# Optimization experiments

Measured on AMD Instinct MI355X. Metric: run time of the kernel, lower is better.

## Reference

```python
import jax, jax.numpy as jnp
import numpy as np
import math

B, L, C_IN = 256, 128, 75
D_EMB = 128      # DataEmbedding d_model
D_MODEL = 126    # encoder d_model (= L-2 after ODConv valid conv k=3)
H = 6
D_HEAD = D_MODEL // H  # 21
D_FF = 2048
FACTOR = 5
K_NUM = 4        # ODConv kernel_num (default)
ATT_CH = 16      # max(int(128*0.0625), 16)
EPS = 1e-5


def _ln(x, g, b):
    m = x.mean(-1, keepdims=True)
    v = ((x - m) ** 2).mean(-1, keepdims=True)
    return (x - m) * jax.lax.rsqrt(v + EPS) * g + b


def _bn_eval(x, g, b):
    # eval-mode BatchNorm, running_mean=0 running_var=1
    return x * (g / np.sqrt(1.0 + EPS)) + b


def _conv1d(x, w, b=None):
    out = jax.lax.conv_general_dilated(x, w, (1,), 'VALID',
                                       dimension_numbers=('NCH', 'OIH', 'NCH'))
    if b is not None:
        out = out + b[None, :, None]
    return out


def _pos_embed(n, d):
    pos = np.arange(n)[:, None].astype(np.float32)
    div = np.exp(np.arange(0, d, 2).astype(np.float32) * (-math.log(10000.0) / d))
    pe = np.zeros((n, d), np.float32)
    pe[:, 0::2] = np.sin(pos * div)
    pe[:, 1::2] = np.cos(pos * div)
    return jnp.asarray(pe)


def _prob_attention(Q, K, V, key):
    # Informer ProbAttention, mask_flag=False. Q,K,V: [B,H,Lq,D]
    b, h, lq, d = Q.shape
    lk = K.shape[2]
    u_keys = min(FACTOR * int(np.ceil(np.log(lk))), lk)
    n_top = min(FACTOR * int(np.ceil(np.log(lq))), lq)
    idx = jax.random.randint(key, (lq, u_keys), 0, lk)     # sampled key ids per query
    K_s = K[:, :, idx, :]                                  # [B,H,Lq,u,D]
    qks = jnp.einsum('bhld,bhlud->bhlu', Q, K_s)
    M = qks.max(-1) - qks.sum(-1) / lk                     # sparsity measure
    _, top = jax.lax.top_k(M, n_top)                       # [B,H,n_top]
    Qr = jnp.take_along_axis(Q, top[..., None], axis=2)    # [B,H,n_top,D]
    scores = jnp.einsum('bhud,bhkd->bhuk', Qr, K) / np.sqrt(d).astype(np.float32)
    upd = jnp.einsum('bhuk,bhkd->bhud', jax.nn.softmax(scores, -1), V)
    ctx = jnp.broadcast_to(V.mean(2, keepdims=True), Q.shape)  # initial context
    bi = jnp.arange(b)[:, None, None]
    hi = jnp.arange(h)[None, :, None]
    return ctx.at[bi, hi, top].set(upd)


def _forward(x_enc, x_mark_enc, token_w, time_w, time_b,
             od_fc_w, od_bn_g, od_bn_b, od_ch_w, od_ch_b, od_fil_w, od_fil_b,
             od_sp_w, od_sp_b, od_ker_w, od_ker_b, od_weight,
             q_w, q_b, k_w, k_b, v_w, v_b, o_w, o_b,
             ffn1_w, ffn1_b, ffn2_w, ffn2_b, ln1_g, ln1_b, ln2_g, ln2_b,
             cl_w, cl_b, cl_bn_g, cl_bn_b, enc_ln_g, enc_ln_b, fc_w, fc_b):
    # ---- DataEmbedding (token circular conv + pos + timeF linear; dropout=eval) ----
    xt = jnp.pad(x_enc.transpose(0, 2, 1), ((0, 0), (0, 0), (1, 1)), mode='wrap')
    tok = _conv1d(xt, token_w).transpose(0, 2, 1)          # [B,L,128]
    emb = tok + _pos_embed(L, D_EMB)[None] + (x_mark_enc @ time_w + time_b)

    # ---- ODConv1d(128,128,k=3,pad=0) on [B,128,L] ----
    x = emb.transpose(0, 2, 1)                             # [B,128,L]
    gap = x.mean(-1)                                       # [B,128]
    a = jax.nn.relu(_bn_eval(gap @ od_fc_w, od_bn_g, od_bn_b))   # [B,16]
    ch_att = jax.nn.sigmoid(a @ od_ch_w + od_ch_b)         # [B,128]
    fil_att = jax.nn.sigmoid(a @ od_fil_w + od_fil_b)      # [B,128]
    sp_att = jax.nn.sigmoid(a @ od_sp_w + od_sp_b)         # [B,3]
    ker_att = jax.nn.softmax(a @ od_ker_w + od_ker_b, -1)  # [B,4]
    xc = x * ch_att[:, :, None]
    agg_w = jnp.einsum('bn,bj,noij->boij', ker_att, sp_att, od_weight)  # [B,128,128,3]
    lout = L - 2
    patches = jnp.stack([xc[:, :, j:j + lout] for j in range(3)], axis=2)  # [B,128,3,126]
    x = jnp.einsum('boij,bijt->bot', agg_w, patches) * fil_att[:, :, None]  # [B,128,126]
    # encoder reads this as (seq=128, d_model=126)

    key = jax.random.key(42)

    def enc_layer(xx, i):
        b, l, _ = xx.shape
        Q = (xx @ q_w[i] + q_b[i]).reshape(b, l, H, D_HEAD).transpose(0, 2, 1, 3)
        Kk = (xx @ k_w[i] + k_b[i]).reshape(b, l, H, D_HEAD).transpose(0, 2, 1, 3)
        Vv = (xx @ v_w[i] + v_b[i]).reshape(b, l, H, D_HEAD).transpose(0, 2, 1, 3)
        ctx = _prob_attention(Q, Kk, Vv, jax.random.fold_in(key, i))
        new_x = ctx.transpose(0, 2, 1, 3).reshape(b, l, D_MODEL) @ o_w[i] + o_b[i]
        xx = _ln(xx + new_x, ln1_g[i], ln1_b[i])
        y = jax.nn.gelu(xx @ ffn1_w[i] + ffn1_b[i], approximate=False)
        y = y @ ffn2_w[i] + ffn2_b[i]
        return _ln(xx + y, ln2_g[i], ln2_b[i])

    x = enc_layer(x, 0)
    # ConvLayer distilling: circular conv k3 + BN + ELU + maxpool(k3,s2,p1): 128 -> 64
    xt = jnp.pad(x.transpose(0, 2, 1), ((0, 0), (0, 0), (1, 1)), mode='wrap')
    xt = _conv1d(xt, cl_w, cl_b)
    xt = jax.nn.elu(_bn_eval(xt, cl_bn_g[None, :, None], cl_bn_b[None, :, None]))
    xt = jax.lax.reduce_window(xt, -jnp.inf, jax.lax.max, (1, 1, 3), (1, 1, 2),
                               [(0, 0), (0, 0), (1, 1)])
    x = xt.transpose(0, 2, 1)                              # [B,64,126]
    x = enc_layer(x, 1)
    x = _ln(x, enc_ln_g, enc_ln_b)

    out = x.transpose(0, 2, 1) @ fc_w + fc_b               # [B,126,1]
    return out.transpose(0, 2, 1)                          # [B,1,126]


def setup_inputs() -> dict:
    key = jax.random.key(0)
    it = iter(jax.random.split(key, 48))
    def rn(shape, s=0.05):
        return jax.random.normal(next(it), shape, dtype=jnp.float32) * s
    return {
        'x_enc': jax.random.normal(next(it), (B, L, C_IN), jnp.float32),
        'x_mark_enc': jax.random.uniform(next(it), (B, L, 3), jnp.float32, -0.5, 0.5),
        'token_w': rn((D_EMB, C_IN, 3), 0.1),
        'time_w': rn((3, D_EMB), 0.1), 'time_b': rn((D_EMB,)),
        'od_fc_w': rn((D_EMB, ATT_CH), 0.1),
        'od_bn_g': jnp.ones((ATT_CH,)), 'od_bn_b': jnp.zeros((ATT_CH,)),
        'od_ch_w': rn((ATT_CH, D_EMB), 0.1), 'od_ch_b': rn((D_EMB,)),
        'od_fil_w': rn((ATT_CH, D_EMB), 0.1), 'od_fil_b': rn((D_EMB,)),
        'od_sp_w': rn((ATT_CH, 3), 0.1), 'od_sp_b': rn((3,)),
        'od_ker_w': rn((ATT_CH, K_NUM), 0.1), 'od_ker_b': rn((K_NUM,)),
        'od_weight': rn((K_NUM, D_EMB, D_EMB, 3), 0.05),
        'q_w': rn((2, D_MODEL, D_MODEL)), 'q_b': rn((2, D_MODEL)),
        'k_w': rn((2, D_MODEL, D_MODEL)), 'k_b': rn((2, D_MODEL)),
        'v_w': rn((2, D_MODEL, D_MODEL)), 'v_b': rn((2, D_MODEL)),
        'o_w': rn((2, D_MODEL, D_MODEL)), 'o_b': rn((2, D_MODEL)),
        'ffn1_w': rn((2, D_MODEL, D_FF), 0.03), 'ffn1_b': rn((2, D_FF)),
        'ffn2_w': rn((2, D_FF, D_MODEL), 0.03), 'ffn2_b': rn((2, D_MODEL)),
        'ln1_g': jnp.ones((2, D_MODEL)), 'ln1_b': jnp.zeros((2, D_MODEL)),
        'ln2_g': jnp.ones((2, D_MODEL)), 'ln2_b': jnp.zeros((2, D_MODEL)),
        'cl_w': rn((D_MODEL, D_MODEL, 3), 0.05), 'cl_b': rn((D_MODEL,)),
        'cl_bn_g': jnp.ones((D_MODEL,)), 'cl_bn_b': jnp.zeros((D_MODEL,)),
        'enc_ln_g': jnp.ones((D_MODEL,)), 'enc_ln_b': jnp.zeros((D_MODEL,)),
        'fc_w': rn((L // 2, 1), 0.1), 'fc_b': rn((1,)),
    }


def reference(x_enc, x_mark_enc, token_w, time_w, time_b,
              od_fc_w, od_bn_g, od_bn_b, od_ch_w, od_ch_b, od_fil_w, od_fil_b,
              od_sp_w, od_sp_b, od_ker_w, od_ker_b, od_weight,
              q_w, q_b, k_w, k_b, v_w, v_b, o_w, o_b,
              ffn1_w, ffn1_b, ffn2_w, ffn2_b, ln1_g, ln1_b, ln2_g, ln2_b,
              cl_w, cl_b, cl_bn_g, cl_bn_b, enc_ln_g, enc_ln_b, fc_w, fc_b):
    return _forward(x_enc, x_mark_enc, token_w, time_w, time_b,
                    od_fc_w, od_bn_g, od_bn_b, od_ch_w, od_ch_b, od_fil_w, od_fil_b,
                    od_sp_w, od_sp_b, od_ker_w, od_ker_b, od_weight,
                    q_w, q_b, k_w, k_b, v_w, v_b, o_w, o_b,
                    ffn1_w, ffn1_b, ffn2_w, ffn2_b, ln1_g, ln1_b, ln2_g, ln2_b,
                    cl_w, cl_b, cl_bn_g, cl_bn_b, enc_ln_g, enc_ln_b, fc_w, fc_b)
```

## Files before the change

kernel.cpp:

```cpp
#include <hip/hip_runtime.h>
#include <math.h>

#define NB 256
#define DM 126
#define DE 128
#define NH 6
#define DHd 21
#define DFF 2048
#define CIN 75
#define L0 128
#define NTOP 25

#ifndef IDX_MODE
#define IDX_MODE 0
#endif

typedef const float* fp;
typedef unsigned short u16;
typedef short s8v __attribute__((ext_vector_type(8)));
typedef float f4v __attribute__((ext_vector_type(4)));

__device__ __forceinline__ u16 f2bf(float x){
  unsigned u = __float_as_uint(x);
  unsigned r = (u + 0x7FFFu + ((u >> 16) & 1u)) >> 16;
  return (u16)r;
}
__device__ __forceinline__ float bf2f(u16 v){
  unsigned uu = ((unsigned)v) << 16;
  return __uint_as_float(uu);
}

__device__ __forceinline__ void gld_lds16(const u16* g, u16* l){
  __builtin_amdgcn_global_load_lds((const __attribute__((address_space(1))) unsigned int*)(const void*)g,
                                   (__attribute__((address_space(3))) unsigned int*)(void*)l,
                                   16, 0, 0);
}

__device__ __forceinline__ unsigned cvt_pk_bf16(float lo, float hi){
  unsigned r;
  asm("v_cvt_pk_bf16_f32 %0, %1, %2" : "=v"(r) : "v"(lo), "v"(hi));
  return r;
}

__device__ __forceinline__ void tf2(unsigned k0, unsigned k1, unsigned x0, unsigned x1,
                                    unsigned &o0, unsigned &o1){
  unsigned ks2 = k0 ^ k1 ^ 0x1BD11BDAu;
  x0 += k0; x1 += k1;
  #define RR(r) { x0 += x1; x1 = (x1 << (r)) | (x1 >> (32 - (r))); x1 ^= x0; }
  RR(13) RR(15) RR(26) RR(6)
  x0 += k1;  x1 += ks2 + 1u;
  RR(17) RR(29) RR(16) RR(24)
  x0 += ks2; x1 += k0 + 2u;
  RR(13) RR(15) RR(26) RR(6)
  x0 += k0;  x1 += k1 + 3u;
  RR(17) RR(29) RR(16) RR(24)
  x0 += k1;  x1 += ks2 + 4u;
  RR(13) RR(15) RR(26) RR(6)
  x0 += ks2; x1 += k0 + 5u;
  #undef RR
  o0 = x0; o1 = x1;
}

__global__ __launch_bounds__(256) void k_zero(float* out, int n){
  int i = blockIdx.x*256 + threadIdx.x;
  if (i < n) out[i] = 0.f;
}

__global__ __launch_bounds__(256) void k_idx(int* idx0, int* idx1){
  int tid = threadIdx.x;
  unsigned a0,a1,c0,c1;
  tf2(0u,42u, 0u,0u, a0,a1);
  tf2(0u,42u, 0u,1u, c0,c1);
  for (int f = tid; f < 3200; f += 256){
    unsigned y0,y1;
#if IDX_MODE==0
    tf2(a0,a1, 0u, (unsigned)(3200+f), y0,y1); idx0[f] = (int)(y1 & 127u);
#elif IDX_MODE==1
    tf2(a0,a1, 0u, (unsigned)(3200+f), y0,y1); idx0[f] = (int)(y0 & 127u);
#elif IDX_MODE==2
    tf2(a0,a1, (unsigned)f, (unsigned)(3200+f), y0,y1); idx0[f] = (int)(y1 & 127u);
#else
    tf2(a0,a1, (unsigned)f, (unsigned)(3200+f), y0,y1); idx0[f] = (int)(y0 & 127u);
#endif
  }
  for (int f = tid; f < 1600; f += 256){
    unsigned y0,y1;
#if IDX_MODE==0
    tf2(c0,c1, 0u, (unsigned)(1600+f), y0,y1); idx1[f] = (int)(y1 & 63u);
#elif IDX_MODE==1
    tf2(c0,c1, 0u, (unsigned)(1600+f), y0,y1); idx1[f] = (int)(y0 & 63u);
#elif IDX_MODE==2
    tf2(c0,c1, (unsigned)f, (unsigned)(1600+f), y0,y1); idx1[f] = (int)(y1 & 63u);
#else
    tf2(c0,c1, (unsigned)f, (unsigned)(1600+f), y0,y1); idx1[f] = (int)(y0 & 63u);
#endif
  }
}

__global__ __launch_bounds__(256) void k_wprep(fp token_w, fp clw,
                                               fp qw, fp qb, fp kw, fp kb, fp vw, fp vb, fp ow,
                                               u16* wemb, u16* wdist, u16* wqkv, u16* wo,
                                               float* qbias){
  int i = blockIdx.x*256 + threadIdx.x;
  if (i < 32768){
    int n = i >> 8, k = i & 255;
    float v = 0.f;
    if (k < 225){ int q = k/75, c = k - q*75; v = token_w[(size_t)n*225 + c*3 + q]; }
    wemb[i] = f2bf(v);
    return;
  }
  i -= 32768;
  if (i < 49152){
    int n = i / 384, k = i - n*384;
    float v = 0.f;
    if (n < DM && k < 378){ int q = k/126, ci = k - q*126; v = clw[((size_t)n*DM + ci)*3 + q]; }
    wdist[i] = f2bf(v);
    return;
  }
  i -= 49152;
  if (i < 2*49152){
    int layer = i / 49152, jj = i - layer*49152;
    int n = jj >> 7, k = jj & 127;
    int sec = n >> 7, nn = n & 127;
    const float* w = (sec == 0) ? qw : ((sec == 1) ? kw : vw);
    float v = (nn < DM && k < DM) ? w[((size_t)layer*DM + k)*DM + nn] : 0.f;
    wqkv[(size_t)layer*49152 + jj] = f2bf(v);
    return;
  }
  i -= 2*49152;
  if (i < 2*16384){
    int layer = i / 16384, jj = i - layer*16384;
    int n = jj >> 7, k = jj & 127;
    float v = (n < DM && k < DM) ? ow[(size_t)layer*DM*DM + k*DM + n] : 0.f;
    wo[(size_t)layer*16384 + jj] = f2bf(v);
    return;
  }
  i -= 2*16384;
  if (i < 768){
    int layer = i / 384, n = i - layer*384;
    int sec = n >> 7, nn = n & 127;
    const float* bp = (sec == 0) ? qb : ((sec == 1) ? kb : vb);
    qbias[(size_t)layer*384 + n] = (nn < DM) ? bp[layer*DM + nn] : 0.f;
  }
}

__global__ __launch_bounds__(256) void k_wtrans(fp f1w, fp f2w, u16* w1t, u16* w2t){
  __shared__ u16 sT[64*65];
  const int t = blockIdx.x;
  const int tid = threadIdx.x, lane = tid & 63, rg = tid >> 6;
  if (t < 128){
    int layer = t >> 6, rem = t & 63;
    int kt = rem >> 5, nt = rem & 31;
    #pragma unroll
    for (int rr = 0; rr < 16; rr++){
      int row = rg + rr*4;
      int k = kt*64 + row;
      float v = (k < DM) ? f1w[((size_t)layer*DM + k)*DFF + nt*64 + lane] : 0.f;
      sT[row*65 + lane] = f2bf(v);
    }
    __syncthreads();
    #pragma unroll
    for (int rr = 0; rr < 16; rr++){
      int nrow = rg + rr*4;
      int n_glob = nt*64 + nrow;
      w1t[(size_t)layer*262144 + (size_t)n_glob*128 + kt*64 + lane] = sT[lane*65 + nrow];
    }
  } else {
    int t2 = t - 128;
    int layer = t2 >> 6, rem = t2 & 63;
    int nt = rem >> 5, ft = rem & 31;
    #pragma unroll
    for (int rr = 0; rr < 16; rr++){
      int row = rg + rr*4;
      int f = ft*64 + row;
      int n = nt*64 + lane;
      float v = (n < DM) ? f2w[((size_t)layer*DFF + f)*DM + n] : 0.f;
      sT[row*65 + lane] = f2bf(v);
    }
    __syncthreads();
    #pragma unroll
    for (int rr = 0; rr < 16; rr++){
      int nrow = rg + rr*4;
      int n_glob = nt*64 + nrow;
      w2t[(size_t)layer*262144 + (size_t)n_glob*2048 + ft*64 + lane] = sT[lane*65 + nrow];
    }
  }
}

__global__ __launch_bounds__(256) void k_front(fp x_enc, fp x_mark, const u16* wemb,
                                               fp time_w, fp time_b,
                                               fp fcw, fp bng, fp bnb,
                                               fp chw, fp chb, fp filw, fp filb,
                                               fp spw, fp spb, fp kerw, fp kerb,
                                               fp odw, float* xout){
  __shared__ __align__(16) u16 smem[71232];
  u16*   sXT = smem;
  u16*   sW  = smem + 17680;
  u16*   sA  = smem + 17680;
  float* sE  = reinterpret_cast<float*>(smem + 17680);
  float* red = reinterpret_cast<float*>(smem + 69904);
  float* gap = reinterpret_cast<float*>(smem + 70416);
  float* aAct= reinterpret_cast<float*>(smem + 70672);
  float* sch = reinterpret_cast<float*>(smem + 70704);
  float* sfil= reinterpret_cast<float*>(smem + 70960);
  float* ssp = reinterpret_cast<float*>(smem + 71216);
  float* sker= reinterpret_cast<float*>(smem + 71224);
  const int tid = threadIdx.x;
  const int wave = tid >> 6, lane = tid & 63, quad = lane >> 4, l15 = lane & 15;
  const int b = blockIdx.x;
  const f4v z4 = {0.f,0.f,0.f,0.f};
  const int mBase = wave * 32;

  {
    const float4* xb = reinterpret_cast<const float4*>(x_enc + (size_t)b*L0*CIN);
    for (int p4 = tid; p4 < (L0*CIN)/4; p4 += 256){
      float4 v4 = xb[p4];
      float vv[4] = {v4.x, v4.y, v4.z, v4.w};
      int e0 = p4*4;
      #pragma unroll
      for (int j = 0; j < 4; j++){
        int e = e0 + j;
        int sr = e / CIN, c = e - sr*CIN;
        u16 bv = f2bf(vv[j]);
        sA[((sr + 1) & 127)*264 + c] = bv;
        sA[sr*264 + 75 + c] = bv;
        sA[((sr + 127) & 127)*264 + 150 + c] = bv;
      }
    }
    for (int p = tid; p < 128*31; p += 256){
      int row = p / 31, c2 = p - row*31;
      sA[row*264 + 225 + c2] = 0;
    }
  }
  __syncthreads();
  {
    f4v acc[2][8];
    #pragma unroll
    for (int m = 0; m < 2; m++)
      #pragma unroll
      for (int t = 0; t < 8; t++) acc[m][t] = z4;
    for (int ks = 0; ks < 8; ks++){
      s8v a0 = *reinterpret_cast<const s8v*>(sA + (mBase + l15)*264 + ks*32 + quad*8);
      s8v a1 = *reinterpret_cast<const s8v*>(sA + (mBase + 16 + l15)*264 + ks*32 + quad*8);
      const u16* wb = wemb + (size_t)l15*256 + ks*32 + quad*8;
      #pragma unroll
      for (int t = 0; t < 8; t++){
        s8v bfr = *reinterpret_cast<const s8v*>(wb + (size_t)t*16*256);
        acc[0][t] = __builtin_amdgcn_mfma_f32_16x16x32_bf16(a0, bfr, acc[0][t], 0, 0, 0);
        acc[1][t] = __builtin_amdgcn_mfma_f32_16x16x32_bf16(a1, bfr, acc[1][t], 0, 0, 0);
      }
    }
    float divc[8], tw0c[8], tw1c[8], tw2c[8], tbc[8];
    #pragma unroll
    for (int t = 0; t < 8; t++){
      int col = t*16 + l15;
      int i2 = col >> 1;
      divc[t] = __expf((float)(2*i2) * (-9.210340371976184f / 128.f));
      tw0c[t] = time_w[col]; tw1c[t] = time_w[128 + col]; tw2c[t] = time_w[256 + col];
      tbc[t] = time_b[col];
    }
    #pragma unroll
    for (int m = 0; m < 2; m++){
      #pragma unroll
      for (int r = 0; r < 4; r++){
        int row = mBase + m*16 + quad*4 + r;
        const float* mk = x_mark + ((size_t)b*L0 + row)*3;
        float m0v = mk[0], m1v = mk[1], m2v = mk[2];
        #pragma unroll
        for (int t = 0; t < 8; t++){
          int col = t*16 + l15;
          float ang = (float)row * divc[t];
          float pe = (col & 1) ? __cosf(ang) : __sinf(ang);
          float tm = m0v*tw0c[t] + m1v*tw1c[t] + m2v*tw2c[t] + tbc[t];
          sE[row*132 + col] = acc[m][t][r] + pe + tm;
        }
      }
    }
  }
  __syncthreads();
  {
    int col = tid & 127, half = tid >> 7;
    float s = 0.f;
    for (int r = 0; r < 64; r++) s += sE[(half*64 + r)*132 + col];
    red[tid] = s;
  }
  __syncthreads();
  if (tid < 128) gap[tid] = (red[tid] + red[tid + 128]) * (1.f/128.f);
  __syncthreads();
  if (tid < 16){
    float acc = 0.f;
    for (int e = 0; e < DE; e++) acc += gap[e]*fcw[e*16 + tid];
    acc = acc * (bng[tid] / sqrtf(1.f + 1e-5f)) + bnb[tid];
    aAct[tid] = fmaxf(acc, 0.f);
  }
  __syncthreads();
  if (tid < 128){
    float accc = 0.f, accf = 0.f;
    for (int c = 0; c < 16; c++){ accc += aAct[c]*chw[c*DE + tid]; accf += aAct[c]*filw[c*DE + tid]; }
    sch[tid]  = 1.f/(1.f + __expf(-(accc + chb[tid])));
    sfil[tid] = 1.f/(1.f + __expf(-(accf + filb[tid])));
  } else if (tid < 131){
    int t = tid - 128;
    float acc = 0.f;
    for (int c = 0; c < 16; c++) acc += aAct[c]*spw[c*3 + t];
    ssp[t] = 1.f/(1.f + __expf(-(acc + spb[t])));
  } else if (tid == 132){
    float v[4]; float mx = -1e30f;
    for (int n = 0; n < 4; n++){
      float acc = 0.f;
      for (int c = 0; c < 16; c++) acc += aAct[c]*kerw[c*4 + n];
      v[n] = acc + kerb[n]; mx = fmaxf(mx, v[n]);
    }
    float ss = 0.f;
    for (int n = 0; n < 4; n++){ v[n] = __expf(v[n]-mx); ss += v[n]; }
    for (int n = 0; n < 4; n++) sker[n] = v[n]/ss;
  }
  __syncthreads();
  for (int p = tid; p < 130*128; p += 256){
    int l = p >> 7, i = p & 127;
    float v = (l < 128) ? sE[l*132 + i]*sch[i] : 0.f;
    sXT[l*136 + i] = f2bf(v);
  }
  __syncthreads();
  {
    float kr0 = sker[0], kr1 = sker[1], kr2 = sker[2], kr3 = sker[3];
    float spq[3]; spq[0] = ssp[0]; spq[1] = ssp[1]; spq[2] = ssp[2];
    const float4* od4 = (const float4*)odw;
    for (int p4 = tid; p4 < 128*384/4; p4 += 256){
      float4 w0 = od4[p4];
      float4 w1 = od4[12288 + p4];
      float4 w2 = od4[24576 + p4];
      float4 w3 = od4[36864 + p4];
      float vv[4] = { kr0*w0.x + kr1*w1.x + kr2*w2.x + kr3*w3.x,
                      kr0*w0.y + kr1*w1.y + kr2*w2.y + kr3*w3.y,
                      kr0*w0.z + kr1*w1.z + kr2*w2.z + kr3*w3.z,
                      kr0*w0.w + kr1*w1.w + kr2*w2.w + kr3*w3.w };
      int e0 = p4*4;
// ... 206 lines not shown
    #pragma unroll
    for (int nt = 0; nt < 2; nt++){
      int d = nt*16 + l15;
      s8v bb;
      if (d < DHd){
        const float* vp = vb + (size_t)d*L + ks*32 + d0;
        #pragma unroll
        for (int j = 0; j < 8; j++) bb[j] = (short)f2bf(vp[j]);
      } else {
        #pragma unroll
        for (int j = 0; j < 8; j++) bb[j] = (short)0;
      }
      s8v a = *reinterpret_cast<const s8v*>(sPb + (mt*16 + l15)*136 + ks*32 + d0);
      pv[nt] = __builtin_amdgcn_mfma_f32_16x16x32_bf16(a, bb, pv[nt], 0, 0, 0);
    }
  }
  #pragma unroll
  for (int nt = 0; nt < 2; nt++){
    #pragma unroll
    for (int r4 = 0; r4 < 4; r4++){
      int u = mt*16 + quad*4 + r4;
      int d = nt*16 + l15;
      if (d < DHd){
        if (u < NTOP)       upd[((size_t)bh*NTOP + u)*DHd + d] = pv[nt][r4];
        else if (u == NTOP) vmean[bh*DHd + d] = pv[nt][r4];
      }
    }
  }
}

__global__ __launch_bounds__(256) void k_oproj_mfma(const float* xin, const float* vmean,
                                                    const int* posmap, const float* upd,
                                                    const u16* wo, fp ob, fp g, fp bb,
                                                    int layer, int lshift, int lmask, float* xmid){
  __shared__ __align__(16) float sOf[64*129];
  __shared__ float prs[128];
  __shared__ float smean[64], srstd[64];
  u16* sX = reinterpret_cast<u16*>(sOf);
  const int tid = threadIdx.x;
  const int wave = tid >> 6, lane = tid & 63, quad = lane >> 4, l15 = lane & 15;
  const int m0 = wave * 16;
  const size_t rows0 = (size_t)blockIdx.x * 64;
  for (int p = tid; p < 64*128; p += 256){
    int r = p >> 7, c = p & 127;
    int gr = (int)rows0 + r, b = gr >> lshift, l = gr & lmask;
    float v = 0.f;
    if (c < DM){
      int h = c / DHd, d = c - h*DHd;
      int bh = b*NH + h;
      int pos = posmap[bh*L0 + l];
      v = (pos >= 0) ? upd[((size_t)bh*NTOP + pos)*DHd + d] : vmean[bh*DHd + d];
    }
    sX[r*136 + c] = f2bf(v);
  }
  __syncthreads();
  const f4v z4 = {0.f,0.f,0.f,0.f};
  f4v acc[8];
  #pragma unroll
  for (int t = 0; t < 8; t++) acc[t] = z4;
  #pragma unroll
  for (int ks = 0; ks < 4; ks++){
    s8v a = *reinterpret_cast<const s8v*>(sX + (m0 + l15)*136 + ks*32 + quad*8);
    const u16* wb = wo + (size_t)l15*128 + ks*32 + quad*8;
    #pragma unroll
    for (int t = 0; t < 8; t++){
      s8v b = *reinterpret_cast<const s8v*>(wb + (size_t)t*16*128);
      acc[t] = __builtin_amdgcn_mfma_f32_16x16x32_bf16(a, b, acc[t], 0, 0, 0);
    }
  }
  __syncthreads();
  #pragma unroll
  for (int t = 0; t < 8; t++){
    int col = t*16 + l15;
    #pragma unroll
    for (int r = 0; r < 4; r++){
      sOf[(m0 + quad*4 + r)*129 + col] = acc[t][r];
    }
  }
  __syncthreads();
  const float* obl = ob + (size_t)layer*DM;
  for (int p = tid; p < 64*DM; p += 256){
    int r = p / DM, c = p - r*DM;
    sOf[r*129 + c] += xin[(rows0 + r)*DM + c] + obl[c];
  }
  __syncthreads();
  if (tid < 128){
    int row = tid >> 1, half = tid & 1;
    float s = 0.f;
    for (int c = half*63; c < half*63 + 63; c++) s += sOf[row*129 + c];
    prs[tid] = s;
  }
  __syncthreads();
  if (tid < 128 && (tid & 1) == 0) smean[tid>>1] = (prs[tid] + prs[tid+1]) / (float)DM;
  __syncthreads();
  if (tid < 128){
    int row = tid >> 1, half = tid & 1;
    float mn = smean[row];
    float s = 0.f;
    for (int c = half*63; c < half*63 + 63; c++){ float d = sOf[row*129 + c] - mn; s += d*d; }
    prs[tid] = s;
  }
  __syncthreads();
  if (tid < 128 && (tid & 1) == 0) srstd[tid>>1] = rsqrtf((prs[tid] + prs[tid+1])/(float)DM + 1e-5f);
  __syncthreads();
  const float* gl = g  + (size_t)layer*DM;
  const float* bl = bb + (size_t)layer*DM;
  for (int p = tid; p < 64*DM; p += 256){
    int r = p / DM, c = p - r*DM;
    xmid[(rows0 + r)*DM + c] = (sOf[r*129 + c] - smean[r])*srstd[r]*gl[c] + bl[c];
  }
}

__device__ __forceinline__ float gelu_fast(float x){
  float x2 = x*x;
  float u = x * __builtin_fmaf(0.10295128f, x2, 2.30212056f);
  u = fminf(u, 126.f);
#if __has_builtin(__builtin_amdgcn_exp2f)
  float t = __builtin_amdgcn_exp2f(u);
#else
  float t = __expf(u * 0.69314718056f);
#endif
  return x * t * __builtin_amdgcn_rcpf(t + 1.f);
}


__device__ __forceinline__ void stage_w1_p(const u16* w1t, int j, u16* buf, int p){
  int n = p >> 4, c = p & 15;
  int cg = c ^ (n & 7);
  gld_lds16(w1t + (((size_t)(j*64 + n)) << 7) + cg*8,
            buf + (size_t)((p >> 6) << 6)*8);
}
__device__ __forceinline__ void stage_w2_p(const u16* w2t, int j, u16* buf, int p){
  int n = p >> 3, c = p & 7;
  int cg = c ^ (n & 7);
  gld_lds16(w2t + (size_t)n*2048 + j*64 + cg*8,
            buf + (size_t)((p >> 6) << 6)*8);
}

__device__ __forceinline__ int yaddr(int row, int col){
  return row*64 + (((col >> 3) ^ (row & 7)) << 3) + (col & 7);
}

__device__ __forceinline__ void lgkm_barrier(){
  asm volatile("s_waitcnt lgkmcnt(0)" ::: "memory");
  __builtin_amdgcn_sched_barrier(0);
  __builtin_amdgcn_s_barrier();
  __builtin_amdgcn_sched_barrier(0);
}

template<int NT>
__global__ __launch_bounds__(NT) void k_ffn(const float* xmid, const u16* w1t, const u16* w2t,
                                            fp b1, fp b2w, fp g, fp bb, int layer,
                                            const u16* wdist, fp e1, fp e2, fp e3, fp e4,
                                            float* out2){
  constexpr int ROWS = NT/8;
  constexpr int NMG  = NT/256;
  constexpr int SYG  = NMG*2048;
  constexpr int SP   = 1024/NT;
  constexpr int SMEMU = (NT == 1024) ? 128*392 : (SYG + 4*8192);
  __shared__ __align__(16) u16 smem[SMEMU];
  __shared__ float prs[2*ROWS];
  __shared__ float smean[ROWS], srstd[ROWS];
  u16* wA0 = smem + SYG;
  u16* wA1 = wA0 + 8192;
  u16* wB0 = wA1 + 8192;
  u16* wB1 = wB0 + 8192;
  const int tid  = threadIdx.x;
  const int wave = tid >> 6, lane = tid & 63, quad = lane >> 4, l15 = lane & 15;
  const int mg = wave >> 2, ng = wave & 3;
  const int rowb = mg * 32;
  u16* sYg = smem + mg*2048;
  const size_t rows0 = (size_t)blockIdx.x * ROWS;

  s8v aX[2][4];
  #pragma unroll
  for (int mt = 0; mt < 2; mt++){
    const float* xr = xmid + (rows0 + rowb + mt*16 + l15)*(size_t)DM;
    #pragma unroll
    for (int ks = 0; ks < 4; ks++){
      #pragma unroll
      for (int j = 0; j < 8; j++){
        int c = ks*32 + quad*8 + j;
        float v = (c < DM) ? xr[c] : 0.f;
        aX[mt][ks][j] = (short)f2bf(v);
      }
    }
  }
  #pragma unroll
  for (int r = 0; r < SP; r++){
    stage_w1_p(w1t, 0, wA0, r*NT + tid);
    stage_w2_p(w2t, 0, wB0, r*NT + tid);
  }

  const float* b1l = b1 + (size_t)layer*DFF;
  const f4v z4 = {0.f, 0.f, 0.f, 0.f};
  f4v acc2[2][2];
  acc2[0][0]=z4; acc2[0][1]=z4; acc2[1][0]=z4; acc2[1][1]=z4;

  for (int j = 0; j < 32; j++){
    u16* wAcur = (j & 1) ? wA1 : wA0;
    u16* wAnxt = (j & 1) ? wA0 : wA1;
    u16* wBcur = (j & 1) ? wB1 : wB0;
    u16* wBnxt = (j & 1) ? wB0 : wB1;
    __syncthreads();
    if (j < 31){
      #pragma unroll
      for (int r = 0; r < SP; r++){
        stage_w1_p(w1t, j+1, wAnxt, r*NT + tid);
        stage_w2_p(w2t, j+1, wBnxt, r*NT + tid);
      }
    }
    f4v acc1[2];
    acc1[0] = z4; acc1[1] = z4;
    {
      int nloc = ng*16 + l15;
      #pragma unroll
      for (int ks = 0; ks < 4; ks++){
        int cg = (ks*4 + quad) ^ (nloc & 7);
        s8v b = *reinterpret_cast<const s8v*>(wAcur + nloc*128 + cg*8);
        acc1[0] = __builtin_amdgcn_mfma_f32_16x16x32_bf16(aX[0][ks], b, acc1[0], 0, 0, 0);
        acc1[1] = __builtin_amdgcn_mfma_f32_16x16x32_bf16(aX[1][ks], b, acc1[1], 0, 0, 0);
      }
    }
    {
      int col = ng*16 + l15;
      float bv = b1l[j*64 + col];
      #pragma unroll
      for (int mt = 0; mt < 2; mt++){
        float y0 = gelu_fast(acc1[mt][0] + bv);
        float y1 = gelu_fast(acc1[mt][1] + bv);
        float y2 = gelu_fast(acc1[mt][2] + bv);
        float y3 = gelu_fast(acc1[mt][3] + bv);
        unsigned p01 = cvt_pk_bf16(y0, y1);
        unsigned p23 = cvt_pk_bf16(y2, y3);
        int r0 = mt*16 + quad*4;
        sYg[yaddr(r0,     col)] = (u16)p01;
        sYg[yaddr(r0 + 1, col)] = (u16)(p01 >> 16);
        sYg[yaddr(r0 + 2, col)] = (u16)p23;
        sYg[yaddr(r0 + 3, col)] = (u16)(p23 >> 16);
      }
    }
    lgkm_barrier();
    #pragma unroll
    for (int ks2 = 0; ks2 < 2; ks2++){
      int ga = ((ks2*4 + quad) ^ (l15 & 7)) << 3;
      s8v a0 = *reinterpret_cast<const s8v*>(sYg + (l15)*64 + ga);
      s8v a1 = *reinterpret_cast<const s8v*>(sYg + (16 + l15)*64 + ga);
      #pragma unroll
      for (int t = 0; t < 2; t++){
        int nloc = ng*32 + t*16 + l15;
        int cg = (ks2*4 + quad) ^ (nloc & 7);
        s8v b = *reinterpret_cast<const s8v*>(wBcur + nloc*64 + cg*8);
        acc2[0][t] = __builtin_amdgcn_mfma_f32_16x16x32_bf16(a0, b, acc2[0][t], 0, 0, 0);
        acc2[1][t] = __builtin_amdgcn_mfma_f32_16x16x32_bf16(a1, b, acc2[1][t], 0, 0, 0);
      }
    }
  }

  __syncthreads();
  float* sO = reinterpret_cast<float*>(smem);
  #pragma unroll
  for (int mt = 0; mt < 2; mt++)
    #pragma unroll
    for (int t = 0; t < 2; t++)
      #pragma unroll
      for (int r = 0; r < 4; r++)
        sO[(rowb + mt*16 + quad*4 + r)*129 + ng*32 + t*16 + l15] = acc2[mt][t][r];
  __syncthreads();
  const float* b2l = b2w + (size_t)layer*DM;
  for (int p = tid; p < ROWS*DM; p += NT){
    int r = p / DM, c = p - r*DM;
    sO[r*129 + c] += b2l[c] + xmid[(rows0 + r)*DM + c];
  }
  __syncthreads();
  if (tid < 2*ROWS){
    int row = tid >> 1, half = tid & 1;
    float s = 0.f;
    for (int c = half*63; c < half*63 + 63; c++) s += sO[row*129 + c];
    prs[tid] = s;
  }
  __syncthreads();
  if (tid < 2*ROWS && (tid & 1) == 0) smean[tid>>1] = (prs[tid] + prs[tid+1]) / (float)DM;
  __syncthreads();
  if (tid < 2*ROWS){
    int row = tid >> 1, half = tid & 1;
    float mn = smean[row];
    float s = 0.f;
    for (int c = half*63; c < half*63 + 63; c++){ float d = sO[row*129 + c] - mn; s += d*d; }
    prs[tid] = s;
  }
  __syncthreads();
  if (tid < 2*ROWS && (tid & 1) == 0) srstd[tid>>1] = rsqrtf((prs[tid] + prs[tid+1])/(float)DM + 1e-5f);
  __syncthreads();
  const float* gl = g  + (size_t)layer*DM;
  const float* bl = bb + (size_t)layer*DM;

  if constexpr (NT == 1024){
    float rv[16];
    #pragma unroll
    for (int k = 0; k < 16; k++){
      int p = tid + k*1024;
      if (p < 128*DM){
        int r = p / DM, c = p - r*DM;
        rv[k] = (sO[r*129 + c] - smean[r])*srstd[r]*gl[c] + bl[c];
      } else rv[k] = 0.f;
    }
    __syncthreads();
    u16* sAd = smem;
    #pragma unroll
    for (int k = 0; k < 16; k++){
      int p = tid + k*1024;
      if (p < 128*DM){
        int r = p / DM, c = p - r*DM;
        u16 bv = f2bf(rv[k]);
        sAd[((r + 1) & 127)*392 + c] = bv;
        sAd[r*392 + 126 + c] = bv;
        sAd[((r + 127) & 127)*392 + 252 + c] = bv;
      }
    }
    if (tid < 768){ int row = tid / 6, c2 = tid - row*6; sAd[row*392 + 378 + c2] = 0; }
    __syncthreads();
    const int mrow  = (wave & 7) * 16;
    const int tbase = (wave >> 3) * 4;
    f4v dac[4];
    dac[0]=z4; dac[1]=z4; dac[2]=z4; dac[3]=z4;
    for (int ks = 0; ks < 12; ks++){
      s8v a = *reinterpret_cast<const s8v*>(sAd + (mrow + l15)*392 + ks*32 + quad*8);
      const u16* wbp = wdist + (size_t)l15*384 + ks*32 + quad*8;
      #pragma unroll
      for (int t = 0; t < 4; t++){
        s8v bfr = *reinterpret_cast<const s8v*>(wbp + (size_t)(tbase + t)*16*384);
        dac[t] = __builtin_amdgcn_mfma_f32_16x16x32_bf16(a, bfr, dac[t], 0, 0, 0);
      }
    }
    __syncthreads();
    float* zsh = reinterpret_cast<float*>(smem);
    const float bnscale = 1.f / sqrtf(1.f + 1e-5f);
    #pragma unroll
    for (int t = 0; t < 4; t++){
      int co = (tbase + t)*16 + l15;
      if (co < DM){
        float cb = e1[co];
        float gg = e2[co] * bnscale, bv = e3[co];
        #pragma unroll
        for (int r = 0; r < 4; r++){
          int row = mrow + quad*4 + r;
          float z = (dac[t][r] + cb)*gg + bv;
          z = (z > 0.f) ? z : (__expf(z) - 1.f);
          zsh[row*130 + co] = z;
        }
      }
    }
    __syncthreads();
    for (int p = tid; p < 64*DM; p += 1024){
      int jj = p / DM, co = p - jj*DM;
      float best = zsh[(2*jj)*130 + co];
      if (jj > 0) best = fmaxf(best, zsh[(2*jj - 1)*130 + co]);
      best = fmaxf(best, zsh[(2*jj + 1)*130 + co]);
      out2[((size_t)blockIdx.x*64 + jj)*DM + co] = best;
    }
  } else {
    for (int p = tid; p < ROWS*DM; p += NT){
      int r = p / DM, c = p - r*DM;
      sO[r*129 + c] = (sO[r*129 + c] - smean[r])*srstd[r]*gl[c] + bl[c];
    }
    __syncthreads();
    if (tid < 2*ROWS){
      int row = tid >> 1, half = tid & 1;
      float s = 0.f;
      for (int c = half*63; c < half*63 + 63; c++) s += sO[row*129 + c];
      prs[tid] = s;
    }
    __syncthreads();
    if (tid < 2*ROWS && (tid & 1) == 0) smean[tid>>1] = (prs[tid] + prs[tid+1]) / (float)DM;
    __syncthreads();
    if (tid < 2*ROWS){
      int row = tid >> 1, half = tid & 1;
      float mn = smean[row];
      float s = 0.f;
      for (int c = half*63; c < half*63 + 63; c++){ float d = sO[row*129 + c] - mn; s += d*d; }
      prs[tid] = s;
    }
    __syncthreads();
    if (tid < 2*ROWS && (tid & 1) == 0) srstd[tid>>1] = rsqrtf((prs[tid] + prs[tid+1])/(float)DM + 1e-5f);
    __syncthreads();
    if (tid < DM){
      float gv = e1[tid], bv2 = e2[tid];
      float acc = e4[0];
      for (int l = 0; l < 64; l++){
        float xn = (sO[l*129 + tid] - smean[l])*srstd[l]*gv + bv2;
        acc += xn * e3[l];
      }
      out2[(size_t)blockIdx.x*DM + tid] = acc;
    }
  }
}

extern "C" void kernel_launch(void* const* d_in, const int* in_sizes, int n_in,
                              void* d_out, int out_size, void* d_ws, size_t ws_size,
                              hipStream_t stream) {
  fp x_enc   = (fp)d_in[0];
  fp x_mark  = (fp)d_in[1];
  fp token_w = (fp)d_in[2];
  fp time_w  = (fp)d_in[3];
  fp time_b  = (fp)d_in[4];
  fp od_fc_w = (fp)d_in[5];
  fp od_bn_g = (fp)d_in[6];
  fp od_bn_b = (fp)d_in[7];
  fp od_ch_w = (fp)d_in[8];
  fp od_ch_b = (fp)d_in[9];
  fp od_fil_w= (fp)d_in[10];
  fp od_fil_b= (fp)d_in[11];
  fp od_sp_w = (fp)d_in[12];
  fp od_sp_b = (fp)d_in[13];
  fp od_ker_w= (fp)d_in[14];
  fp od_ker_b= (fp)d_in[15];
  fp od_wt   = (fp)d_in[16];
  fp q_w = (fp)d_in[17]; fp q_b = (fp)d_in[18];
  fp k_w = (fp)d_in[19]; fp k_b = (fp)d_in[20];
  fp v_w = (fp)d_in[21]; fp v_b = (fp)d_in[22];
  fp o_w = (fp)d_in[23]; fp o_b = (fp)d_in[24];
  fp f1w = (fp)d_in[25]; fp f1b = (fp)d_in[26];
  fp f2w = (fp)d_in[27]; fp f2b = (fp)d_in[28];
  fp ln1g= (fp)d_in[29]; fp ln1b= (fp)d_in[30];
  fp ln2g= (fp)d_in[31]; fp ln2b= (fp)d_in[32];
  fp cl_w= (fp)d_in[33]; fp cl_b= (fp)d_in[34];
  fp clbg= (fp)d_in[35]; fp clbb= (fp)d_in[36];
  fp elng= (fp)d_in[37]; fp elnb= (fp)d_in[38];
  fp fc_w= (fp)d_in[39]; fp fc_b= (fp)d_in[40];

  const size_t OFF_IDX0 = 0;
  const size_t OFF_IDX1 = OFF_IDX0 + 3200;
  const size_t OFF_CH   = OFF_IDX1 + 1600;
  const size_t OFF_FIL  = OFF_CH  + (size_t)NB*DE;
  const size_t OFF_SP   = OFF_FIL + (size_t)NB*DE;
  const size_t OFF_KER  = OFF_SP  + (size_t)NB*4;
  const size_t OFF_VM   = OFF_KER + (size_t)NB*4;
  const size_t OFF_POS  = OFF_VM  + (size_t)NB*NH*DHd;
  const size_t OFF_UPD  = OFF_POS + (size_t)NB*NH*L0;
  const size_t OFF_STOP = OFF_UPD + (size_t)NB*NH*NTOP*DHd;
  const size_t OFF_WTS  = (OFF_STOP + (size_t)NB*NH*NTOP + 255) & ~(size_t)255;
  const size_t WTS_FLOATS = (2*262144 + 2*262144 + 2*49152 + 2*16384 + 49152 + 32768)/2 + 2*384;
  const size_t OFF_BIG  = (OFF_WTS + WTS_FLOATS + 255) & ~(size_t)255;
  const size_t SBUF     = (size_t)NB*DE*L0;
  const size_t TOTAL    = OFF_BIG + 4*SBUF;

  if (ws_size < TOTAL*sizeof(float)){
    hipLaunchKernelGGL(k_zero, dim3((out_size+255)/256), dim3(256), 0, stream,
                       (float*)d_out, out_size);
    return;
  }

  float* ws = (float*)d_ws;
  int* idx0 = (int*)(ws + OFF_IDX0);
  int* idx1 = (int*)(ws + OFF_IDX1);
  float* vme = ws + OFF_VM;
  int* posm  = (int*)(ws + OFF_POS);
  float* updb= ws + OFF_UPD;
  u16* w1tb  = (u16*)(ws + OFF_WTS);
  u16* w2tb  = w1tb + 2*262144;
  u16* wqkvb = w2tb + 2*262144;
  u16* wob   = wqkvb + 2*49152;
  u16* wdistb= wob + 2*16384;
  u16* wembb = wdistb + 49152;
  float* qkvbias = (float*)(wembb + 32768);

  float* X    = ws + OFF_BIG;
  float* QKV  = X + SBUF;
  float* VT   = X + 3*SBUF;
  float* xmid = QKV;

  hipLaunchKernelGGL(k_idx, dim3(1), dim3(256), 0, stream, idx0, idx1);
  hipLaunchKernelGGL(k_wprep, dim3(835), dim3(256), 0, stream,
                     token_w, cl_w, q_w, q_b, k_w, k_b, v_w, v_b, o_w,
                     wembb, wdistb, wqkvb, wob, qkvbias);
  hipLaunchKernelGGL(k_wtrans, dim3(256), dim3(256), 0, stream,
                     f1w, f2w, w1tb, w2tb);
  hipLaunchKernelGGL(k_front, dim3(NB), dim3(256), 0, stream,
                     x_enc, x_mark, wembb, time_w, time_b,
                     od_fc_w, od_bn_g, od_bn_b, od_ch_w, od_ch_b, od_fil_w, od_fil_b,
                     od_sp_w, od_sp_b, od_ker_w, od_ker_b, od_wt, X);

  hipLaunchKernelGGL(k_qkv_mfma, dim3(NB*L0/64), dim3(256), 0, stream,
                     X, wqkvb, qkvbias, QKV, VT, 128, 7, 127);
  hipLaunchKernelGGL(k_attn, dim3(NB*NH), dim3(128), 0, stream,
                     QKV, VT, idx0, L0, posm, vme, updb);
  hipLaunchKernelGGL(k_oproj_mfma, dim3(NB*L0/64), dim3(256), 0, stream,
                     X, vme, posm, updb, wob, o_b, ln1g, ln1b, 0, 7, 127, xmid);
  hipLaunchKernelGGL((k_ffn<1024>), dim3(NB), dim3(1024), 0, stream,
                     xmid, w1tb, w2tb, f1b, f2b, ln2g, ln2b, 0,
                     wdistb, cl_b, clbg, clbb, cl_b, X);

  hipLaunchKernelGGL(k_qkv_mfma, dim3(NB*64/64), dim3(256), 0, stream,
                     X, wqkvb + 49152, qkvbias + 384, QKV, VT, 64, 6, 63);
  hipLaunchKernelGGL(k_attn, dim3(NB*NH), dim3(128), 0, stream,
                     QKV, VT, idx1, 64, posm, vme, updb);
  hipLaunchKernelGGL(k_oproj_mfma, dim3(NB*64/64), dim3(256), 0, stream,
                     X, vme, posm, updb, wob + 16384, o_b, ln1g, ln1b, 1, 6, 63, xmid);
  hipLaunchKernelGGL((k_ffn<512>), dim3(256), dim3(512), 0, stream,
                     xmid, w1tb + 262144, w2tb + 262144, f1b, f2b, ln2g, ln2b, 1,
                     wdistb, elng, elnb, fc_w, fc_b, (float*)d_out);
  (void)in_sizes; (void)n_in; (void)out_size; (void)ws_size;
}
```

Before: 592.2 us.

## Fuse layer-0 output projection and LayerNorm into FFN kernel, merge prep kernels

Merges the three weight/index preparation kernels into one launch with block-range dispatch. Folds the layer-0 attention output projection, residual add and LayerNorm1 into the 1024-thread FFN kernel, so its input stays in shared memory instead of going through a global xmid buffer. The layer-0 output goes to a separate buffer X2, because the fused kernel still reads X as the residual. This removes two kernel launches and a global round trip, but enlarges the FFN kernel's shared memory footprint and serialises the projection inside each block.

```diff
diff --git a/kernel.cpp b/kernel.cpp
--- a/kernel.cpp
+++ b/kernel.cpp
@@ -66,123 +66,128 @@
   if (i < n) out[i] = 0.f;
 }
 
-__global__ __launch_bounds__(256) void k_idx(int* idx0, int* idx1){
-  int tid = threadIdx.x;
-  unsigned a0,a1,c0,c1;
-  tf2(0u,42u, 0u,0u, a0,a1);
-  tf2(0u,42u, 0u,1u, c0,c1);
-  for (int f = tid; f < 3200; f += 256){
-    unsigned y0,y1;
+__global__ __launch_bounds__(256) void k_prep(int* idx0, int* idx1,
+                                              fp token_w, fp clw,
+                                              fp qw, fp qb, fp kw, fp kb, fp vw, fp vb, fp ow,
+                                              u16* wemb, u16* wdist, u16* wqkv, u16* wo,
+                                              float* qbias,
+                                              fp f1w, fp f2w, u16* w1t, u16* w2t){
+  __shared__ u16 sT[64*65];
+  const int blk = blockIdx.x;
+  const int tid = threadIdx.x;
+  if (blk == 0){
+    unsigned a0,a1,c0,c1;
+    tf2(0u,42u, 0u,0u, a0,a1);
+    tf2(0u,42u, 0u,1u, c0,c1);
+    for (int f = tid; f < 3200; f += 256){
+      unsigned y0,y1;
 #if IDX_MODE==0
-    tf2(a0,a1, 0u, (unsigned)(3200+f), y0,y1); idx0[f] = (int)(y1 & 127u);
+      tf2(a0,a1, 0u, (unsigned)(3200+f), y0,y1); idx0[f] = (int)(y1 & 127u);
 #elif IDX_MODE==1
-    tf2(a0,a1, 0u, (unsigned)(3200+f), y0,y1); idx0[f] = (int)(y0 & 127u);
+      tf2(a0,a1, 0u, (unsigned)(3200+f), y0,y1); idx0[f] = (int)(y0 & 127u);
 #elif IDX_MODE==2
-    tf2(a0,a1, (unsigned)f, (unsigned)(3200+f), y0,y1); idx0[f] = (int)(y1 & 127u);
+      tf2(a0,a1, (unsigned)f, (unsigned)(3200+f), y0,y1); idx0[f] = (int)(y1 & 127u);
 #else
-    tf2(a0,a1, (unsigned)f, (unsigned)(3200+f), y0,y1); idx0[f] = (int)(y0 & 127u);
+      tf2(a0,a1, (unsigned)f, (unsigned)(3200+f), y0,y1); idx0[f] = (int)(y0 & 127u);
 #endif
-  }
-  for (int f = tid; f < 1600; f += 256){
-    unsigned y0,y1;
+    }
+    for (int f = tid; f < 1600; f += 256){
+      unsigned y0,y1;
 #if IDX_MODE==0
-    tf2(c0,c1, 0u, (unsigned)(1600+f), y0,y1); idx1[f] = (int)(y1 & 63u);
+      tf2(c0,c1, 0u, (unsigned)(1600+f), y0,y1); idx1[f] = (int)(y1 & 63u);
 #elif IDX_MODE==1
-    tf2(c0,c1, 0u, (unsigned)(1600+f), y0,y1); idx1[f] = (int)(y0 & 63u);
+      tf2(c0,c1, 0u, (unsigned)(1600+f), y0,y1); idx1[f] = (int)(y0 & 63u);
 #elif IDX_MODE==2
-    tf2(c0,c1, (unsigned)f, (unsigned)(1600+f), y0,y1); idx1[f] = (int)(y1 & 63u);
+      tf2(c0,c1, (unsigned)f, (unsigned)(1600+f), y0,y1); idx1[f] = (int)(y1 & 63u);
 #else
-    tf2(c0,c1, (unsigned)f, (unsigned)(1600+f), y0,y1); idx1[f] = (int)(y0 & 63u);
+      tf2(c0,c1, (unsigned)f, (unsigned)(1600+f), y0,y1); idx1[f] = (int)(y0 & 63u);
 #endif
-  }
-}
-
-__global__ __launch_bounds__(256) void k_wprep(fp token_w, fp clw,
-                                               fp qw, fp qb, fp kw, fp kb, fp vw, fp vb, fp ow,
-                                               u16* wemb, u16* wdist, u16* wqkv, u16* wo,
-                                               float* qbias){
-  int i = blockIdx.x*256 + threadIdx.x;
-  if (i < 32768){
-    int n = i >> 8, k = i & 255;
-    float v = 0.f;
-    if (k < 225){ int q = k/75, c = k - q*75; v = token_w[(size_t)n*225 + c*3 + q]; }
-    wemb[i] = f2bf(v);
+    }
     return;
   }
-  i -= 32768;
-  if (i < 49152){
-    int n = i / 384, k = i - n*384;
-    float v = 0.f;
-    if (n < DM && k < 378){ int q = k/126, ci = k - q*126; v = clw[((size_t)n*DM + ci)*3 + q]; }
-    wdist[i] = f2bf(v);
+  if (blk <= 835){
+    int i = (blk - 1)*256 + tid;
+    if (i < 32768){
+      int n = i >> 8, k = i & 255;
+      float v = 0.f;
+      if (k < 225){ int q = k/75, c = k - q*75; v = token_w[(size_t)n*225 + c*3 + q]; }
+      wemb[i] = f2bf(v);
+      return;
+    }
+    i -= 32768;
+    if (i < 49152){
+      int n = i / 384, k = i - n*384;
+      float v = 0.f;
+      if (n < DM && k < 378){ int q = k/126, ci = k - q*126; v = clw[((size_t)n*DM + ci)*3 + q]; }
+      wdist[i] = f2bf(v);
+      return;
+    }
+    i -= 49152;
+    if (i < 2*49152){
+      int layer = i / 49152, jj = i - layer*49152;
+      int n = jj >> 7, k = jj & 127;
+      int sec = n >> 7, nn = n & 127;
+      const float* w = (sec == 0) ? qw : ((sec == 1) ? kw : vw);
+      float v = (nn < DM && k < DM) ? w[((size_t)layer*DM + k)*DM + nn] : 0.f;
+      wqkv[(size_t)layer*49152 + jj] = f2bf(v);
+      return;
+    }
+    i -= 2*49152;
+    if (i < 2*16384){
+      int layer = i / 16384, jj = i - layer*16384;
+      int n = jj >> 7, k = jj & 127;
+      float v = (n < DM && k < DM) ? ow[(size_t)layer*DM*DM + k*DM + n] : 0.f;
+      wo[(size_t)layer*16384 + jj] = f2bf(v);
+      return;
+    }
+    i -= 2*16384;
+    if (i < 768){
+      int layer = i / 384, n = i - layer*384;
+      int sec = n >> 7, nn = n & 127;
+      const float* bp = (sec == 0) ? qb : ((sec == 1) ? kb : vb);
+      qbias[(size_t)layer*384 + n] = (nn < DM) ? bp[layer*DM + nn] : 0.f;
+    }
     return;
   }
-  i -= 49152;
-  if (i < 2*49152){
-    int layer = i / 49152, jj = i - layer*49152;
-    int n = jj >> 7, k = jj & 127;
-    int sec = n >> 7, nn = n & 127;
-    const float* w = (sec == 0) ? qw : ((sec == 1) ? kw : vw);
-    float v = (nn < DM && k < DM) ? w[((size_t)layer*DM + k)*DM + nn] : 0.f;
-    wqkv[(size_t)layer*49152 + jj] = f2bf(v);
-    return;
-  }
-  i -= 2*49152;
-  if (i < 2*16384){
-    int layer = i / 16384, jj = i - layer*16384;
-    int n = jj >> 7, k = jj & 127;
-    float v = (n < DM && k < DM) ? ow[(size_t)layer*DM*DM + k*DM + n] : 0.f;
-    wo[(size_t)layer*16384 + jj] = f2bf(v);
-    return;
-  }
-  i -= 2*16384;
-  if (i < 768){
-    int layer = i / 384, n = i - layer*384;
-    int sec = n >> 7, nn = n & 127;
-    const float* bp = (sec == 0) ? qb : ((sec == 1) ? kb : vb);
-    qbias[(size_t)layer*384 + n] = (nn < DM) ? bp[layer*DM + nn] : 0.f;
-  }
-}
-
-__global__ __launch_bounds__(256) void k_wtrans(fp f1w, fp f2w, u16* w1t, u16* w2t){
-  __shared__ u16 sT[64*65];
-  const int t = blockIdx.x;
-  const int tid = threadIdx.x, lane = tid & 63, rg = tid >> 6;
-  if (t < 128){
-    int layer = t >> 6, rem = t & 63;
-    int kt = rem >> 5, nt = rem & 31;
-    #pragma unroll
-    for (int rr = 0; rr < 16; rr++){
-      int row = rg + rr*4;
-      int k = kt*64 + row;
-      float v = (k < DM) ? f1w[((size_t)layer*DM + k)*DFF + nt*64 + lane] : 0.f;
-      sT[row*65 + lane] = f2bf(v);
-    }
-    __syncthreads();
-    #pragma unroll
-    for (int rr = 0; rr < 16; rr++){
-      int nrow = rg + rr*4;
-      int n_glob = nt*64 + nrow;
-      w1t[(size_t)layer*262144 + (size_t)n_glob*128 + kt*64 + lane] = sT[lane*65 + nrow];
-    }
-  } else {
-    int t2 = t - 128;
-    int layer = t2 >> 6, rem = t2 & 63;
-    int nt = rem >> 5, ft = rem & 31;
-    #pragma unroll
-    for (int rr = 0; rr < 16; rr++){
-      int row = rg + rr*4;
-      int f = ft*64 + row;
-      int n = nt*64 + lane;
-      float v = (n < DM) ? f2w[((size_t)layer*DFF + f)*DM + n] : 0.f;
-      sT[row*65 + lane] = f2bf(v);
-    }
-    __syncthreads();
-    #pragma unroll
-    for (int rr = 0; rr < 16; rr++){
-      int nrow = rg + rr*4;
-      int n_glob = nt*64 + nrow;
-      w2t[(size_t)layer*262144 + (size_t)n_glob*2048 + ft*64 + lane] = sT[lane*65 + nrow];
+  {
+    const int t = blk - 836;
+    const int lane = tid & 63, rg = tid >> 6;
+    if (t < 128){
+      int layer = t >> 6, rem = t & 63;
+      int kt = rem >> 5, nt = rem & 31;
+      #pragma unroll
+      for (int rr = 0; rr < 16; rr++){
+        int row = rg + rr*4;
+        int k = kt*64 + row;
+        float v = (k < DM) ? f1w[((size_t)layer*DM + k)*DFF + nt*64 + lane] : 0.f;
+        sT[row*65 + lane] = f2bf(v);
+      }
+      __syncthreads();
+      #pragma unroll
+      for (int rr = 0; rr < 16; rr++){
+        int nrow = rg + rr*4;
+        int n_glob = nt*64 + nrow;
+        w1t[(size_t)layer*262144 + (size_t)n_glob*128 + kt*64 + lane] = sT[lane*65 + nrow];
+      }
+    } else {
+      int t2 = t - 128;
+      int layer = t2 >> 6, rem = t2 & 63;
+      int nt = rem >> 5, ft = rem & 31;
+      #pragma unroll
+      for (int rr = 0; rr < 16; rr++){
+        int row = rg + rr*4;
+        int f = ft*64 + row;
+        int n = nt*64 + lane;
+        float v = (n < DM) ? f2w[((size_t)layer*DFF + f)*DM + n] : 0.f;
+        sT[row*65 + lane] = f2bf(v);
+      }
+      __syncthreads();
+      #pragma unroll
+      for (int rr = 0; rr < 16; rr++){
+        int nrow = rg + rr*4;
+        int n_glob = nt*64 + nrow;
+        w2t[(size_t)layer*262144 + (size_t)n_glob*2048 + ft*64 + lane] = sT[lane*65 + nrow];
+      }
     }
   }
 }
@@ -695,12 +700,16 @@
 __global__ __launch_bounds__(NT) void k_ffn(const float* xmid, const u16* w1t, const u16* w2t,
                                             fp b1, fp b2w, fp g, fp bb, int layer,
                                             const u16* wdist, fp e1, fp e2, fp e3, fp e4,
+                                            const float* xres, const float* vmeanp,
+                                            const int* posmapp, const float* updp,
+                                            const u16* wo, fp obp, fp l1g, fp l1b,
                                             float* out2){
   constexpr int ROWS = NT/8;
   constexpr int NMG  = NT/256;
   constexpr int SYG  = NMG*2048;
   constexpr int SP   = 1024/NT;
-  constexpr int SMEMU = (NT == 1024) ? 128*392 : (SYG + 4*8192);
+  constexpr int XMOFF = SYG + 4*8192;
+  constexpr int SMEMU = (NT == 1024) ? (XMOFF + 128*130*2) : (SYG + 4*8192);
   __shared__ __align__(16) u16 smem[SMEMU];
   __shared__ float prs[2*ROWS];
   __shared__ float smean[ROWS], srstd[ROWS];
@@ -714,18 +723,93 @@
   const int rowb = mg * 32;
   u16* sYg = smem + mg*2048;
   const size_t rows0 = (size_t)blockIdx.x * ROWS;
+  const f4v z4 = {0.f, 0.f, 0.f, 0.f};
+  float* xm = reinterpret_cast<float*>(smem + XMOFF);
+
+  if constexpr (NT == 1024){
+    const int bb_ = blockIdx.x;
+    u16* sX = smem;
+    for (int p = tid; p < 128*128; p += 1024){
+      int r = p >> 7, c = p & 127;
+      float v = 0.f;
+      if (c < DM){
+        int h = c / DHd, d = c - h*DHd;
+        int bh = bb_*NH + h;
+        int pos = posmapp[bh*L0 + r];
+        v = (pos >= 0) ? updp[((size_t)bh*NTOP + pos)*DHd + d] : vmeanp[bh*DHd + d];
+      }
+      sX[r*136 + c] = f2bf(v);
+    }
+    __syncthreads();
+    const int m0o = (wave & 7) * 16;
+    const int nb0 = (wave >> 3) * 4;
+    f4v oacc[4];
+    oacc[0]=z4; oacc[1]=z4; oacc[2]=z4; oacc[3]=z4;
+    #pragma unroll
+    for (int ks = 0; ks < 4; ks++){
+      s8v a = *reinterpret_cast<const s8v*>(sX + (m0o + l15)*136 + ks*32 + quad*8);
+      const u16* wbp = wo + (size_t)l15*128 + ks*32 + quad*8;
+      #pragma unroll
+      for (int t = 0; t < 4; t++){
+        s8v bfr = *reinterpret_cast<const s8v*>(wbp + (size_t)(nb0 + t)*16*128);
+        oacc[t] = __builtin_amdgcn_mfma_f32_16x16x32_bf16(a, bfr, oacc[t], 0, 0, 0);
+      }
+    }
+    __syncthreads();
+    float* sOf = reinterpret_cast<float*>(smem);
+    #pragma unroll
+    for (int t = 0; t < 4; t++){
+      int col = (nb0 + t)*16 + l15;
+      #pragma unroll
+      for (int r = 0; r < 4; r++)
+        sOf[(m0o + quad*4 + r)*129 + col] = oacc[t][r];
+    }
+    __syncthreads();
+    for (int p = tid; p < 128*DM; p += 1024){
+      int r = p / DM, c = p - r*DM;
+      sOf[r*129 + c] += xres[((size_t)bb_*128 + r)*DM + c] + obp[c];
+    }
+    __syncthreads();
+    if (tid < 256){
+      int row = tid >> 1, half = tid & 1;
+      float s = 0.f;
+      for (int c = half*63; c < half*63 + 63; c++) s += sOf[row*129 + c];
+      prs[tid] = s;
+    }
+    __syncthreads();
+    if (tid < 256 && (tid & 1) == 0) smean[tid>>1] = (prs[tid] + prs[tid+1]) / (float)DM;
+    __syncthreads();
+    if (tid < 256){
+      int row = tid >> 1, half = tid & 1;
+      float mn = smean[row];
+      float s = 0.f;
+      for (int c = half*63; c < half*63 + 63; c++){ float d = sOf[row*129 + c] - mn; s += d*d; }
+      prs[tid] = s;
+    }
+    __syncthreads();
+    if (tid < 256 && (tid & 1) == 0) srstd[tid>>1] = rsqrtf((prs[tid] + prs[tid+1])/(float)DM + 1e-5f);
+    __syncthreads();
+    for (int p = tid; p < 128*DM; p += 1024){
+      int r = p / DM, c = p - r*DM;
+      xm[r*130 + c] = (sOf[r*129 + c] - smean[r])*srstd[r]*l1g[c] + l1b[c];
+    }
+    __syncthreads();
+  }
 
   s8v aX[2][4];
   #pragma unroll
   for (int mt = 0; mt < 2; mt++){
-    const float* xr = xmid + (rows0 + rowb + mt*16 + l15)*(size_t)DM;
     #pragma unroll
     for (int ks = 0; ks < 4; ks++){
       #pragma unroll
-      for (int j = 0; j < 8; j++){
-        int c = ks*32 + quad*8 + j;
-        float v = (c < DM) ? xr[c] : 0.f;
-        aX[mt][ks][j] = (short)f2bf(v);
+      for (int jj2 = 0; jj2 < 8; jj2++){
+        int c = ks*32 + quad*8 + jj2;
+        float v = 0.f;
+        if (c < DM){
+          if constexpr (NT == 1024) v = xm[(rowb + mt*16 + l15)*130 + c];
+          else v = xmid[(rows0 + rowb + mt*16 + l15)*(size_t)DM + c];
+        }
+        aX[mt][ks][jj2] = (short)f2bf(v);
       }
     }
   }
@@ -736,7 +820,6 @@
   }
 
   const float* b1l = b1 + (size_t)layer*DFF;
-  const f4v z4 = {0.f, 0.f, 0.f, 0.f};
   f4v acc2[2][2];
   acc2[0][0]=z4; acc2[0][1]=z4; acc2[1][0]=z4; acc2[1][1]=z4;
 
@@ -813,7 +896,10 @@
   const float* b2l = b2w + (size_t)layer*DM;
   for (int p = tid; p < ROWS*DM; p += NT){
     int r = p / DM, c = p - r*DM;
-    sO[r*129 + c] += b2l[c] + xmid[(rows0 + r)*DM + c];
+    float res;
+    if constexpr (NT == 1024) res = xm[r*130 + c];
+    else res = xmid[(rows0 + r)*DM + c];
+    sO[r*129 + c] += b2l[c] + res;
   }
   __syncthreads();
   if (tid < 2*ROWS){
@@ -1010,14 +1096,13 @@
 
   float* X    = ws + OFF_BIG;
   float* QKV  = X + SBUF;
+  float* X2   = X + 2*SBUF;
   float* VT   = X + 3*SBUF;
   float* xmid = QKV;
 
-  hipLaunchKernelGGL(k_idx, dim3(1), dim3(256), 0, stream, idx0, idx1);
-  hipLaunchKernelGGL(k_wprep, dim3(835), dim3(256), 0, stream,
-                     token_w, cl_w, q_w, q_b, k_w, k_b, v_w, v_b, o_w,
-                     wembb, wdistb, wqkvb, wob, qkvbias);
-  hipLaunchKernelGGL(k_wtrans, dim3(256), dim3(256), 0, stream,
+  hipLaunchKernelGGL(k_prep, dim3(1092), dim3(256), 0, stream,
+                     idx0, idx1, token_w, cl_w, q_w, q_b, k_w, k_b, v_w, v_b, o_w,
+                     wembb, wdistb, wqkvb, wob, qkvbias,
                      f1w, f2w, w1tb, w2tb);
   hipLaunchKernelGGL(k_front, dim3(NB), dim3(256), 0, stream,
                      x_enc, x_mark, wembb, time_w, time_b,
@@ -1028,20 +1113,22 @@
                      X, wqkvb, qkvbias, QKV, VT, 128, 7, 127);
   hipLaunchKernelGGL(k_attn, dim3(NB*NH), dim3(128), 0, stream,
                      QKV, VT, idx0, L0, posm, vme, updb);
-  hipLaunchKernelGGL(k_oproj_mfma, dim3(NB*L0/64), dim3(256), 0, stream,
-                     X, vme, posm, updb, wob, o_b, ln1g, ln1b, 0, 7, 127, xmid);
   hipLaunchKernelGGL((k_ffn<1024>), dim3(NB), dim3(1024), 0, stream,
-                     xmid, w1tb, w2tb, f1b, f2b, ln2g, ln2b, 0,
-                     wdistb, cl_b, clbg, clbb, cl_b, X);
+                     X, w1tb, w2tb, f1b, f2b, ln2g, ln2b, 0,
+                     wdistb, cl_b, clbg, clbb, cl_b,
+                     X, vme, posm, updb, wob, o_b, ln1g, ln1b,
+                     X2);
 
   hipLaunchKernelGGL(k_qkv_mfma, dim3(NB*64/64), dim3(256), 0, stream,
-                     X, wqkvb + 49152, qkvbias + 384, QKV, VT, 64, 6, 63);
+                     X2, wqkvb + 49152, qkvbias + 384, QKV, VT, 64, 6, 63);
   hipLaunchKernelGGL(k_attn, dim3(NB*NH), dim3(128), 0, stream,
                      QKV, VT, idx1, 64, posm, vme, updb);
   hipLaunchKernelGGL(k_oproj_mfma, dim3(NB*64/64), dim3(256), 0, stream,
-                     X, vme, posm, updb, wob + 16384, o_b, ln1g, ln1b, 1, 6, 63, xmid);
+                     X2, vme, posm, updb, wob + 16384, o_b, ln1g, ln1b, 1, 6, 63, xmid);
   hipLaunchKernelGGL((k_ffn<512>), dim3(256), dim3(512), 0, stream,
                      xmid, w1tb + 262144, w2tb + 262144, f1b, f2b, ln2g, ln2b, 1,
-                     wdistb, elng, elnb, fc_w, fc_b, (float*)d_out);
+                     wdistb, elng, elnb, fc_w, fc_b,
+                     X2, vme, posm, updb, wob, o_b, ln1g, ln1b,
+                     (float*)d_out);
   (void)in_sizes; (void)n_in; (void)out_size; (void)ws_size;
 }
```

Result: faster. 564.3 us (-4.7%).
